# Optimization experiments

Measured on AMD Instinct MI355X. Metric: run time of the kernel, lower is better.

Reference implementation:

```python
import jax, jax.numpy as jnp
import numpy as np

N = 80000   # nodes
E = 320000  # directed edges
B = 3200    # graphs (25 nodes each)
D = 256     # emb_dim
L = 5       # num_layer
SIZES = [121, 8, 12, 15, 10, 9, 7, 3, 3]          # atom-feature vocab sizes
ESIZES = [25, 6, 2]                               # bond-feature vocab sizes
OFFS = np.concatenate([[0], np.cumsum(SIZES)[:-1]])  # offsets into fused node table
BN_EPS = 1e-5


def setup_inputs() -> dict:
    key = jax.random.key(0)
    ks = jax.random.split(key, 32)
    # int node features, per-column vocab bound
    x = jnp.stack([jax.random.randint(ks[i], (N,), 0, SIZES[i]) for i in range(9)], axis=1)
    edge_index = jax.random.randint(ks[9], (2, E), 0, N)
    edge_attr = jnp.stack([jax.random.randint(ks[10 + j], (E,), 0, ESIZES[j]) for j in range(3)], axis=1)
    batch = jnp.arange(N) // (N // B)  # sorted graph ids, 25 nodes per graph
    s = 0.1
    node_emb = jax.random.normal(ks[13], (int(sum(SIZES)), D)) * s  # fused 9 tables
    edge_emb1 = jax.random.normal(ks[14], (L, 25, D)) * s
    edge_emb2 = jax.random.normal(ks[15], (L, 6, D)) * s
    edge_emb3 = jax.random.normal(ks[16], (L, 2, D)) * s
    w = 0.05
    W1 = jax.random.normal(ks[17], (L, D, 2 * D)) * w
    b1 = jnp.zeros((L, 2 * D))
    W2 = jax.random.normal(ks[18], (L, 2 * D, D)) * w
    b2 = jnp.zeros((L, D))
    bn_g = jnp.ones((L, D))
    bn_b = jnp.zeros((L, D))
    H = D // 2
    HW1 = jax.random.normal(ks[19], (D, H)) * w
    Hb1 = jnp.zeros((H,))
    HW2 = jax.random.normal(ks[20], (H, H)) * w
    Hb2 = jnp.zeros((H,))
    HW3 = jax.random.normal(ks[21], (H, 2)) * w
    Hb3 = jnp.zeros((2,))
    return {"x": x, "edge_index": edge_index, "edge_attr": edge_attr, "batch": batch,
            "node_emb": node_emb, "edge_emb1": edge_emb1, "edge_emb2": edge_emb2,
            "edge_emb3": edge_emb3, "W1": W1, "b1": b1, "W2": W2, "b2": b2,
            "bn_g": bn_g, "bn_b": bn_b, "HW1": HW1, "Hb1": Hb1, "HW2": HW2,
            "Hb2": Hb2, "HW3": HW3, "Hb3": Hb3}


def _gnn_graphpred(x, edge_index, edge_attr, batch, node_emb, edge_emb1, edge_emb2,
                   edge_emb3, W1, b1, W2, b2, bn_g, bn_b, HW1, Hb1, HW2, Hb2, HW3, Hb3):
    n = x.shape[0]
    offs = jnp.asarray(OFFS, dtype=x.dtype)
    # sum of 9 atom embeddings == one gather into fused table
    h = node_emb[x + offs[None, :]].sum(axis=1)            # [N, D]
    # add self loops; self-loop edge_attr = [22, 0, 0]
    loop = jnp.arange(n, dtype=edge_index.dtype)
    src = jnp.concatenate([edge_index[0], loop])
    dst = jnp.concatenate([edge_index[1], loop])
    ea0 = jnp.concatenate([edge_attr[:, 0], jnp.full((n,), 22, edge_attr.dtype)])
    ea1 = jnp.concatenate([edge_attr[:, 1], jnp.zeros((n,), edge_attr.dtype)])
    ea2 = jnp.concatenate([edge_attr[:, 2], jnp.zeros((n,), edge_attr.dtype)])
    nl = W1.shape[0]
    relu_flag = jnp.arange(nl) < (nl - 1)   # ReLU on all but last layer (JK='last')

    def layer(hc, p):
        e1, e2, e3, w1, bb1, w2, bb2, g, b, flag = p
        eemb = e1[ea0] + e2[ea1] + e3[ea2]                 # [E+N, D]
        msg = hc[src] + eemb                                # gather + add
        aggr = jax.ops.segment_sum(msg, dst, num_segments=n)  # scatter-sum
        h2 = jax.nn.relu(aggr @ w1 + bb1) @ w2 + bb2        # GIN MLP
        mean = h2.mean(axis=0)
        var = h2.var(axis=0)                                # BatchNorm (batch stats)
        h2 = (h2 - mean) * jax.lax.rsqrt(var + BN_EPS) * g + b
        h2 = jnp.where(flag, jax.nn.relu(h2), h2)
        return h2, None

    h, _ = jax.lax.scan(layer, h, (edge_emb1, edge_emb2, edge_emb3, W1, b1, W2, b2,
                                   bn_g, bn_b, relu_flag))
    # super_node_rep: last node of each graph (batch is sorted)
    last_idx = jax.ops.segment_max(jnp.arange(n), batch, num_segments=B)
    super_rep = h[last_idx]                                 # [B, D]
    z = jax.nn.elu(super_rep @ HW1 + Hb1)
    z = jax.nn.elu(z @ HW2 + Hb2)
    return z @ HW3 + Hb3                                    # [B, 2]


def reference(x, edge_index, edge_attr, batch, node_emb, edge_emb1, edge_emb2,
              edge_emb3, W1, b1, W2, b2, bn_g, bn_b, HW1, Hb1, HW2, Hb2, HW3, Hb3):
    return _gnn_graphpred(x, edge_index, edge_attr, batch, node_emb, edge_emb1,
                          edge_emb2, edge_emb3, W1, b1, W2, b2, bn_g, bn_b,
                          HW1, Hb1, HW2, Hb2, HW3, Hb3)
```

## Files before the change

kernel.cpp:

```cpp
#include <hip/hip_runtime.h>
#include <hip/hip_bf16.h>

#define NN 80000
#define EE 320000
#define ET 400000
#define BB 3200
#define LL 5
#define NBLK 313

typedef __attribute__((ext_vector_type(8))) short bf16x8;
typedef __attribute__((ext_vector_type(8))) unsigned short u16x8;
typedef __attribute__((ext_vector_type(4))) float f32x4;

__device__ __forceinline__ float bf2f(unsigned short u) {
    unsigned int v = ((unsigned int)u) << 16;
    return __builtin_bit_cast(float, v);
}
__device__ __forceinline__ unsigned short f2bf(float f) {
    return __builtin_bit_cast(unsigned short, __float2bfloat16(f));
}


__global__ void k_deg(const int* ei, int* deg) {
    int e = blockIdx.x * 256 + threadIdx.x;
    if (e >= ET) return;
    int d = (e < EE) ? ei[EE + e] : (e - EE);
    atomicAdd(&deg[d], 1);
}

__global__ void k_scan1(const int* deg, int* blksum) {
    __shared__ int sh[256];
    int t = threadIdx.x, b = blockIdx.x;
    int i = b * 256 + t;
    int v = (i < NN) ? deg[i] : 0;
    sh[t] = v; __syncthreads();
    for (int off = 128; off > 0; off >>= 1) {
        if (t < off) sh[t] += sh[t + off];
        __syncthreads();
    }
    if (t == 0) blksum[b] = sh[0];
}

__global__ __launch_bounds__(512) void k_scan2(const int* blksum, int* blkoff) {
    __shared__ int sh[512];
    int t = threadIdx.x;
    int v = (t < NBLK) ? blksum[t] : 0;
    sh[t] = v; __syncthreads();
    for (int off = 1; off < 512; off <<= 1) {
        int x = (t >= off) ? sh[t - off] : 0;
        __syncthreads();
        sh[t] += x;
        __syncthreads();
    }
    if (t < NBLK) blkoff[t] = sh[t] - v;
}

__global__ void k_scan3(const int* deg, const int* blkoff, int* row_start, int* cursor) {
    __shared__ int sh[256];
    int t = threadIdx.x, b = blockIdx.x;
    int i = b * 256 + t;
    int v = (i < NN) ? deg[i] : 0;
    sh[t] = v; __syncthreads();
    for (int off = 1; off < 256; off <<= 1) {
        int x = (t >= off) ? sh[t - off] : 0;
        __syncthreads();
        sh[t] += x;
        __syncthreads();
    }
    int exc = sh[t] - v + blkoff[b];
    if (i < NN) { row_start[i] = exc; cursor[i] = exc; }
    if (i == NN - 1) row_start[NN] = exc + v;
}

__global__ void k_fill(const int* ei, const int* ea, int* cursor, int* eid, int* combo) {
    int e = blockIdx.x * 256 + threadIdx.x;
    if (e >= ET) return;
    int d = (e < EE) ? ei[EE + e] : (e - EE);
    int p = atomicAdd(&cursor[d], 1);
    eid[p] = e;
    int c;
    if (e < EE) c = ea[e * 3 + 0] * 12 + ea[e * 3 + 1] * 2 + ea[e * 3 + 2];
    else        c = 22 * 12;
    combo[e] = c;
}

__global__ void k_sortbkt(const int* row_start, int* eid) {
    int v = blockIdx.x * 256 + threadIdx.x;
    if (v >= NN) return;
    int s0 = row_start[v], s1 = row_start[v + 1];
    for (int i = s0 + 1; i < s1; i++) {
        int key = eid[i];
        int j = i - 1;
        while (j >= s0 && eid[j] > key) { eid[j + 1] = eid[j]; j--; }
        eid[j + 1] = key;
    }
}

__global__ void k_remap(const int* eid, const int* combo, const int* ei_src,
                        int* csrc, int* ccomb) {
    int p = blockIdx.x * 256 + threadIdx.x;
    if (p >= ET) return;
    int e = eid[p];
    csrc[p]  = (e < EE) ? ei_src[e] : (e - EE);
    ccomb[p] = combo[e];
}

__global__ void k_ecomb(const float* e1, const float* e2, const float* e3, float* ec) {
    int l = blockIdx.x / 300, c = blockIdx.x % 300, d = threadIdx.x;
    int a0 = c / 12, a1 = (c / 2) % 6, a2 = c & 1;
    ec[(size_t)(l * 300 + c) * 256 + d] =
        e1[(size_t)(l * 25 + a0) * 256 + d] +
        e2[(size_t)(l * 6 + a1) * 256 + d] +
        e3[(size_t)(l * 2 + a2) * 256 + d];
}

__global__ void k_w1t(const float* W, __hip_bfloat16* Wt) {
    int i = blockIdx.x * 256 + threadIdx.x;
    if (i >= LL * 512 * 256) return;
    int l = i / (512 * 256); int r = i % (512 * 256); int n = r / 256; int k = r % 256;
    Wt[i] = __float2bfloat16(W[(size_t)(l * 256 + k) * 512 + n]);
}
__global__ void k_w2t(const float* W, __hip_bfloat16* Wt) {
    int i = blockIdx.x * 256 + threadIdx.x;
    if (i >= LL * 256 * 512) return;
    int l = i / (256 * 512); int r = i % (256 * 512); int n = r / 512; int k = r % 512;
    Wt[i] = __float2bfloat16(W[(size_t)(l * 512 + k) * 256 + n]);
}

__global__ void k_nodeemb(const int* x, const float* emb, __hip_bfloat16* h) {
    const int offs[9] = {0, 121, 129, 141, 156, 166, 175, 182, 185};
    int i = blockIdx.x; int d = threadIdx.x;
    float acc = 0.f;
#pragma unroll
    for (int c = 0; c < 9; c++) {
        int idx = x[i * 9 + c] + offs[c];
        acc += emb[(size_t)idx * 256 + d];
    }
    h[(size_t)i * 256 + d] = __float2bfloat16(acc);
}


__global__ __launch_bounds__(256) void k_aggr(const __hip_bfloat16* h, const float* ecomb_l,
        const int* row_start, const int* csrc, const int* ccomb,
        __hip_bfloat16* aggrB) {
    int wid = threadIdx.x >> 6;
    int lane = threadIdx.x & 63;
    int v = blockIdx.x * 8 + wid * 2 + (lane >> 5);
    int sl = lane & 31;
    int s0 = row_start[v], s1 = row_start[v + 1];
    const unsigned short* hp = (const unsigned short*)h;
    float acc[8] = {0.f, 0.f, 0.f, 0.f, 0.f, 0.f, 0.f, 0.f};
    for (int p = s0; p < s1; p++) {
        int s = csrc[p];
        int c = ccomb[p];
        u16x8 hv = *(const u16x8*)(hp + (size_t)s * 256 + sl * 8);
        f32x4 e0 = *(const f32x4*)(ecomb_l + (size_t)c * 256 + sl * 8);
        f32x4 e1 = *(const f32x4*)(ecomb_l + (size_t)c * 256 + sl * 8 + 4);
        acc[0] += bf2f(hv[0]) + e0.x;
        acc[1] += bf2f(hv[1]) + e0.y;
        acc[2] += bf2f(hv[2]) + e0.z;
        acc[3] += bf2f(hv[3]) + e0.w;
        acc[4] += bf2f(hv[4]) + e1.x;
        acc[5] += bf2f(hv[5]) + e1.y;
        acc[6] += bf2f(hv[6]) + e1.z;
        acc[7] += bf2f(hv[7]) + e1.w;
    }
    u16x8 o;
#pragma unroll
    for (int j = 0; j < 8; j++) o[j] = f2bf(acc[j]);
    *(u16x8*)((unsigned short*)aggrB + (size_t)v * 256 + sl * 8) = o;
}

template<int K, bool RELU, bool OUTBF, bool STATS>
__global__ __launch_bounds__(256) void k_gemm(const __hip_bfloat16* A, const __hip_bfloat16* Wt,
                                              const float* bias, void* out, int Nn,
                                              float* psum, float* psq) {
    __shared__ short lA[2][128 * 32];
    __shared__ short lB[2][128 * 32];
    __shared__ float redS[4][64], redQ[4][64];
    int tid = threadIdx.x;
    int wave = tid >> 6, lane = tid & 63;
    int mBase = blockIdx.x * 128;
    int nBase = blockIdx.y * 128;
    int wr = (wave >> 1) * 64;
    int wc = (wave & 1) * 64;
    int lr = lane & 15, lk = lane >> 4;
    const short* Ap = (const short*)A + (size_t)mBase * K;
    const short* Bp = (const short*)Wt + (size_t)nBase * K;
    int srow = lane >> 2;
    int sslot = lane & 3;
    f32x4 acc[4][4] = {};
    constexpr int NT = K / 32;

    auto stage = [&](int buf, int k0) {
#pragma unroll
        for (int i = 0; i < 2; i++) {
            int chunk = wave * 2 + i;
            int r = chunk * 16 + srow;
            int scol = (sslot ^ ((r ^ (r >> 2)) & 3)) * 8;
            __builtin_amdgcn_global_load_lds(
                (const __attribute__((address_space(1))) unsigned int*)(Ap + (size_t)r * K + k0 + scol),
                (__attribute__((address_space(3))) unsigned int*)(&lA[buf][chunk * 512]), 16, 0, 0);
            __builtin_amdgcn_global_load_lds(
                (const __attribute__((address_space(1))) unsigned int*)(Bp + (size_t)r * K + k0 + scol),
                (__attribute__((address_space(3))) unsigned int*)(&lB[buf][chunk * 512]), 16, 0, 0);
        }
    };

    stage(0, 0);
    __syncthreads();

    for (int t = 0; t < NT; t++) {
        int cur = t & 1;
        if (t + 1 < NT) stage(cur ^ 1, (t + 1) * 32);
        bf16x8 a[4], b[4];
#pragma unroll
        for (int m = 0; m < 4; m++) {
            int r = wr + m * 16 + lr;
            a[m] = *(const bf16x8*)(&lA[cur][r * 32 + ((lk ^ ((r ^ (r >> 2)) & 3)) << 3)]);
        }
#pragma unroll
        for (int n = 0; n < 4; n++) {
            int r = wc + n * 16 + lr;
            b[n] = *(const bf16x8*)(&lB[cur][r * 32 + ((lk ^ ((r ^ (r >> 2)) & 3)) << 3)]);
        }
#pragma unroll
        for (int m = 0; m < 4; m++)
#pragma unroll
            for (int n = 0; n < 4; n++)
                acc[m][n] = __builtin_amdgcn_mfma_f32_16x16x32_bf16(a[m], b[n], acc[m][n], 0, 0, 0);
        __syncthreads();
    }

    float colS[4] = {0.f, 0.f, 0.f, 0.f}, colQ[4] = {0.f, 0.f, 0.f, 0.f};
#pragma unroll
    for (int m = 0; m < 4; m++)
#pragma unroll
        for (int n = 0; n < 4; n++) {
            int cdx = nBase + wc + n * 16 + lr;
            float bi = bias[cdx];
#pragma unroll
            for (int j = 0; j < 4; j++) {
                int r = mBase + wr + m * 16 + lk * 4 + j;
                float v = acc[m][n][j] + bi;
                if (RELU) v = fmaxf(v, 0.f);
                if (OUTBF) ((__hip_bfloat16*)out)[(size_t)r * Nn + cdx] = __float2bfloat16(v);
                else       ((float*)out)[(size_t)r * Nn + cdx] = v;
                if (STATS) { colS[n] += v; colQ[n] += v * v; }
            }
        }

    if (STATS) {
#pragma unroll
        for (int n = 0; n < 4; n++) {
            for (int off = 16; off < 64; off <<= 1) {
                colS[n] += __shfl_xor(colS[n], off);
                colQ[n] += __shfl_xor(colQ[n], off);
            }
        }
        if (lk == 0) {
#pragma unroll
            for (int n = 0; n < 4; n++) {
                redS[wave][n * 16 + lr] = colS[n];
                redQ[wave][n * 16 + lr] = colQ[n];
            }
        }
        __syncthreads();
        if (tid < 128) {
            int c = tid;
            int w0 = (c < 64) ? 0 : 1;
            int cc = c & 63;
            float S = redS[w0][cc] + redS[w0 + 2][cc];
            float Q = redQ[w0][cc] + redQ[w0 + 2][cc];
            psum[(size_t)(nBase + c) * 625 + blockIdx.x] = S;
            psq [(size_t)(nBase + c) * 625 + blockIdx.x] = Q;
        }
    }
}

__global__ __launch_bounds__(256) void k_bn2(const float* psum, const float* psq,
                                             const float* g, const float* bta, float* stat) {
    __shared__ float s1[256], s2[256];
    int d = blockIdx.x; int t = threadIdx.x;
    float a = 0.f, b = 0.f;
    for (int rb = t; rb < 625; rb += 256) {
        a += psum[(size_t)d * 625 + rb];
        b += psq [(size_t)d * 625 + rb];
    }
    s1[t] = a; s2[t] = b; __syncthreads();
    for (int off = 128; off > 0; off >>= 1) {
        if (t < off) { s1[t] += s1[t + off]; s2[t] += s2[t + off]; }
        __syncthreads();
    }
    if (t == 0) {
        float mean = s1[0] / NN;
        float var = s2[0] / NN - mean * mean;
        float sc = rsqrtf(var + 1e-5f) * g[d];
        stat[d] = sc;
        stat[256 + d] = bta[d] - mean * sc;
    }
}

__global__ void k_bnapply(const float* h2, const float* stat, __hip_bfloat16* h, int relu) {
    int i = (blockIdx.x * 256 + threadIdx.x) * 4;
    int d = i & 255;
    f32x4 v = *(const f32x4*)(h2 + i);
    f32x4 sc = *(const f32x4*)(stat + d);
    f32x4 sh = *(const f32x4*)(stat + 256 + d);
    float r0 = v.x * sc.x + sh.x;
    float r1 = v.y * sc.y + sh.y;
    float r2 = v.z * sc.z + sh.z;
    float r3 = v.w * sc.w + sh.w;
    if (relu) {
        r0 = fmaxf(r0, 0.f); r1 = fmaxf(r1, 0.f);
        r2 = fmaxf(r2, 0.f); r3 = fmaxf(r3, 0.f);
    }
    ushort4 o;
    o.x = f2bf(r0); o.y = f2bf(r1); o.z = f2bf(r2); o.w = f2bf(r3);
    *(ushort4*)((unsigned short*)h + i) = o;
}

__global__ __launch_bounds__(128) void k_head(const float* h2, const float* stat,
        const float* HW1, const float* Hb1, const float* HW2, const float* Hb2,
        const float* HW3, const float* Hb3, float* out) {
    __shared__ float row[256], z1[128], z2[128];
    int g = blockIdx.x; int t = threadIdx.x;
    size_t node = (size_t)g * 25 + 24;
    row[t]       = h2[node * 256 + t] * stat[t] + stat[256 + t];
    row[t + 128] = h2[node * 256 + t + 128] * stat[t + 128] + stat[256 + t + 128];
    __syncthreads();
    float acc = Hb1[t];
    for (int k = 0; k < 256; k++) acc += row[k] * HW1[k * 128 + t];
    z1[t] = acc > 0.f ? acc : expm1f(acc);
    __syncthreads();
    acc = Hb2[t];
    for (int k = 0; k < 128; k++) acc += z1[k] * HW2[k * 128 + t];
    z2[t] = acc > 0.f ? acc : expm1f(acc);
    __syncthreads();
    if (t < 2) {
        acc = Hb3[t];
        for (int k = 0; k < 128; k++) acc += z2[k] * HW3[k * 2 + t];
        out[g * 2 + t] = acc;
    }
}


extern "C" void kernel_launch(void* const* d_in, const int* in_sizes, int n_in,
                              void* d_out, int out_size, void* d_ws, size_t ws_size,
                              hipStream_t stream) {
    const int* x          = (const int*)d_in[0];
    const int* edge_index = (const int*)d_in[1];
    const int* edge_attr  = (const int*)d_in[2];
    const float* node_emb = (const float*)d_in[4];
    const float* ee1 = (const float*)d_in[5];
    const float* ee2 = (const float*)d_in[6];
    const float* ee3 = (const float*)d_in[7];
    const float* W1  = (const float*)d_in[8];
    const float* b1  = (const float*)d_in[9];
    const float* W2  = (const float*)d_in[10];
    const float* b2  = (const float*)d_in[11];
    const float* bng = (const float*)d_in[12];
    const float* bnb = (const float*)d_in[13];
    const float* HW1 = (const float*)d_in[14];
    const float* Hb1 = (const float*)d_in[15];
    const float* HW2 = (const float*)d_in[16];
    const float* Hb2 = (const float*)d_in[17];
    const float* HW3 = (const float*)d_in[18];
    const float* Hb3 = (const float*)d_in[19];
    float* out = (float*)d_out;

    char* ws = (char*)d_ws;
    size_t off = 0;
    auto alloc = [&](size_t bytes) -> char* {
        off = (off + 255) & ~(size_t)255;
        char* p = ws + off;
        off += bytes;
        return p;
    };
    int* deg       = (int*)alloc((size_t)NN * 4);
    int* cursor    = (int*)alloc((size_t)NN * 4);
    int* row_start = (int*)alloc((size_t)(NN + 1) * 4);
    int* blksum    = (int*)alloc((size_t)(NBLK + 1) * 4);
    int* blkoff    = (int*)alloc((size_t)(NBLK + 1) * 4);
    int* eid       = (int*)alloc((size_t)ET * 4);
    int* combo     = (int*)alloc((size_t)ET * 4);
    int* csrc      = (int*)alloc((size_t)ET * 4);
    int* ccomb     = (int*)alloc((size_t)ET * 4);
    float* ecomb   = (float*)alloc((size_t)LL * 300 * 256 * 4);
    __hip_bfloat16* W1t = (__hip_bfloat16*)alloc((size_t)LL * 512 * 256 * 2);
    __hip_bfloat16* W2t = (__hip_bfloat16*)alloc((size_t)LL * 256 * 512 * 2);
    __hip_bfloat16* h    = (__hip_bfloat16*)alloc((size_t)NN * 256 * 2);
    __hip_bfloat16* aggrB = (__hip_bfloat16*)alloc((size_t)NN * 256 * 2);
    __hip_bfloat16* act  = (__hip_bfloat16*)alloc((size_t)NN * 512 * 2);
    float* h2     = (float*)alloc((size_t)NN * 256 * 4);
    float* psum   = (float*)alloc((size_t)256 * 625 * 4);
    float* psq    = (float*)alloc((size_t)256 * 625 * 4);
    float* bnstat = (float*)alloc((size_t)512 * 4);

    hipMemsetAsync(deg, 0, (size_t)NN * 4, stream);
    k_deg<<<(ET + 255) / 256, 256, 0, stream>>>(edge_index, deg);
    k_scan1<<<NBLK, 256, 0, stream>>>(deg, blksum);
    k_scan2<<<1, 512, 0, stream>>>(blksum, blkoff);
    k_scan3<<<NBLK, 256, 0, stream>>>(deg, blkoff, row_start, cursor);
    k_fill<<<(ET + 255) / 256, 256, 0, stream>>>(edge_index, edge_attr, cursor, eid, combo);
    k_sortbkt<<<(NN + 255) / 256, 256, 0, stream>>>(row_start, eid);
    k_remap<<<(ET + 255) / 256, 256, 0, stream>>>(eid, combo, edge_index, csrc, ccomb);
    k_ecomb<<<LL * 300, 256, 0, stream>>>(ee1, ee2, ee3, ecomb);
    k_w1t<<<(LL * 512 * 256 + 255) / 256, 256, 0, stream>>>(W1, W1t);
    k_w2t<<<(LL * 256 * 512 + 255) / 256, 256, 0, stream>>>(W2, W2t);
    k_nodeemb<<<NN, 256, 0, stream>>>(x, node_emb, h);

    for (int l = 0; l < LL; l++) {
        k_aggr<<<NN / 8, 256, 0, stream>>>(h, ecomb + (size_t)l * 300 * 256, row_start,
                                           csrc, ccomb, aggrB);
        k_gemm<256, true, true, false><<<dim3(625, 4), 256, 0, stream>>>(
            aggrB, W1t + (size_t)l * 512 * 256, b1 + l * 512, act, 512, nullptr, nullptr);
        k_gemm<512, false, false, true><<<dim3(625, 2), 256, 0, stream>>>(
            act, W2t + (size_t)l * 256 * 512, b2 + l * 256, h2, 256, psum, psq);
        k_bn2<<<256, 256, 0, stream>>>(psum, psq, bng + l * 256, bnb + l * 256, bnstat);
        if (l < LL - 1)
            k_bnapply<<<NN * 256 / (256 * 4), 256, 0, stream>>>(h2, bnstat, h, 1);
    }

    k_head<<<BB, 128, 0, stream>>>(h2, bnstat, HW1, Hb1, HW2, Hb2, HW3, Hb3, out);
}
```

Baseline: 944.3 us.

## Fuse GIN MLP GEMMs into one kernel with split-bf16 weights

Replaces the two separate GEMM launches per layer with one kernel. Each block computes a 64-row tile of the first GEMM and keeps the ReLU activation in swizzled LDS, then runs the second GEMM from LDS, so the 512-wide activation no longer round-trips through global memory. Weights are split into bf16 hi and lo parts, which doubles the MFMA count to recover fp32-like weight precision. The B operands are now read directly from global memory without LDS staging, which may cost bandwidth. The last layer writes h2 only for the rows the head reads.

```diff
diff --git a/kernel.cpp b/kernel.cpp
--- a/kernel.cpp
+++ b/kernel.cpp
@@ -7,6 +7,7 @@
 #define BB 3200
 #define LL 5
 #define NBLK 313
+#define MLPB 1250
 
 typedef __attribute__((ext_vector_type(8))) short bf16x8;
 typedef __attribute__((ext_vector_type(8))) unsigned short u16x8;
@@ -114,17 +115,23 @@
         e3[(size_t)(l * 2 + a2) * 256 + d];
 }
 
-__global__ void k_w1t(const float* W, __hip_bfloat16* Wt) {
+__global__ void k_w1t(const float* W, __hip_bfloat16* Whi, __hip_bfloat16* Wlo) {
     int i = blockIdx.x * 256 + threadIdx.x;
     if (i >= LL * 512 * 256) return;
     int l = i / (512 * 256); int r = i % (512 * 256); int n = r / 256; int k = r % 256;
-    Wt[i] = __float2bfloat16(W[(size_t)(l * 256 + k) * 512 + n]);
-}
-__global__ void k_w2t(const float* W, __hip_bfloat16* Wt) {
+    float w = W[(size_t)(l * 256 + k) * 512 + n];
+    unsigned short hi = f2bf(w);
+    Whi[i] = __float2bfloat16(w);
+    Wlo[i] = __float2bfloat16(w - bf2f(hi));
+}
+__global__ void k_w2t(const float* W, __hip_bfloat16* Whi, __hip_bfloat16* Wlo) {
     int i = blockIdx.x * 256 + threadIdx.x;
     if (i >= LL * 256 * 512) return;
     int l = i / (256 * 512); int r = i % (256 * 512); int n = r / 512; int k = r % 512;
-    Wt[i] = __float2bfloat16(W[(size_t)(l * 512 + k) * 256 + n]);
+    float w = W[(size_t)(l * 512 + k) * 256 + n];
+    unsigned short hi = f2bf(w);
+    Whi[i] = __float2bfloat16(w);
+    Wlo[i] = __float2bfloat16(w - bf2f(hi));
 }
 
 __global__ void k_nodeemb(const int* x, const float* emb, __hip_bfloat16* h) {
@@ -171,109 +178,112 @@
     *(u16x8*)((unsigned short*)aggrB + (size_t)v * 256 + sl * 8) = o;
 }
 
-template<int K, bool RELU, bool OUTBF, bool STATS>
-__global__ __launch_bounds__(256) void k_gemm(const __hip_bfloat16* A, const __hip_bfloat16* Wt,
-                                              const float* bias, void* out, int Nn,
-                                              float* psum, float* psq) {
-    __shared__ short lA[2][128 * 32];
-    __shared__ short lB[2][128 * 32];
-    __shared__ float redS[4][64], redQ[4][64];
+template<bool LAST>
+__global__ __launch_bounds__(512) void k_mlp(const __hip_bfloat16* aggrB,
+        const __hip_bfloat16* W1hi, const __hip_bfloat16* W1lo, const float* b1v,
+        const __hip_bfloat16* W2hi, const __hip_bfloat16* W2lo, const float* b2v,
+        float* h2, float* psum, float* psq) {
+    __shared__ short sAct[64 * 512];
     int tid = threadIdx.x;
     int wave = tid >> 6, lane = tid & 63;
-    int mBase = blockIdx.x * 128;
-    int nBase = blockIdx.y * 128;
-    int wr = (wave >> 1) * 64;
-    int wc = (wave & 1) * 64;
     int lr = lane & 15, lk = lane >> 4;
-    const short* Ap = (const short*)A + (size_t)mBase * K;
-    const short* Bp = (const short*)Wt + (size_t)nBase * K;
-    int srow = lane >> 2;
-    int sslot = lane & 3;
-    f32x4 acc[4][4] = {};
-    constexpr int NT = K / 32;
-
-    auto stage = [&](int buf, int k0) {
-#pragma unroll
-        for (int i = 0; i < 2; i++) {
-            int chunk = wave * 2 + i;
-            int r = chunk * 16 + srow;
-            int scol = (sslot ^ ((r ^ (r >> 2)) & 3)) * 8;
-            __builtin_amdgcn_global_load_lds(
-                (const __attribute__((address_space(1))) unsigned int*)(Ap + (size_t)r * K + k0 + scol),
-                (__attribute__((address_space(3))) unsigned int*)(&lA[buf][chunk * 512]), 16, 0, 0);
-            __builtin_amdgcn_global_load_lds(
-                (const __attribute__((address_space(1))) unsigned int*)(Bp + (size_t)r * K + k0 + scol),
-                (__attribute__((address_space(3))) unsigned int*)(&lB[buf][chunk * 512]), 16, 0, 0);
-        }
-    };
-
-    stage(0, 0);
+    int mBase = blockIdx.x * 64;
+
+    const short* Ap  = (const short*)aggrB + (size_t)mBase * 256;
+    const short* B1h = (const short*)W1hi + (size_t)(wave * 64) * 256;
+    const short* B1l = (const short*)W1lo + (size_t)(wave * 64) * 256;
+    f32x4 acc1[4][4] = {};
+#pragma unroll 1
+    for (int t = 0; t < 8; t++) {
+        int k0 = t * 32;
+        bf16x8 a[4], bh[4], bl[4];
+#pragma unroll
+        for (int m = 0; m < 4; m++)
+            a[m] = *(const bf16x8*)(Ap + (size_t)(m * 16 + lr) * 256 + k0 + lk * 8);
+#pragma unroll
+        for (int n = 0; n < 4; n++) {
+            bh[n] = *(const bf16x8*)(B1h + (size_t)(n * 16 + lr) * 256 + k0 + lk * 8);
+            bl[n] = *(const bf16x8*)(B1l + (size_t)(n * 16 + lr) * 256 + k0 + lk * 8);
+        }
+#pragma unroll
+        for (int m = 0; m < 4; m++)
+#pragma unroll
+            for (int n = 0; n < 4; n++) {
+                acc1[m][n] = __builtin_amdgcn_mfma_f32_16x16x32_bf16(a[m], bh[n], acc1[m][n], 0, 0, 0);
+                acc1[m][n] = __builtin_amdgcn_mfma_f32_16x16x32_bf16(a[m], bl[n], acc1[m][n], 0, 0, 0);
+            }
+    }
+#pragma unroll
+    for (int m = 0; m < 4; m++)
+#pragma unroll
+        for (int n = 0; n < 4; n++) {
+            int col = wave * 64 + n * 16 + lr;
+            float bi = b1v[col];
+            int cb = col >> 3, ci = col & 7;
+#pragma unroll
+            for (int j = 0; j < 4; j++) {
+                int row = m * 16 + lk * 4 + j;
+                float v = fmaxf(acc1[m][n][j] + bi, 0.f);
+                sAct[row * 512 + ((cb ^ (row & 7)) << 3) + ci] = (short)f2bf(v);
+            }
+        }
     __syncthreads();
 
-    for (int t = 0; t < NT; t++) {
-        int cur = t & 1;
-        if (t + 1 < NT) stage(cur ^ 1, (t + 1) * 32);
-        bf16x8 a[4], b[4];
+    const short* B2h = (const short*)W2hi + (size_t)(wave * 32) * 512;
+    const short* B2l = (const short*)W2lo + (size_t)(wave * 32) * 512;
+    f32x4 acc2[4][2] = {};
+#pragma unroll 1
+    for (int t = 0; t < 16; t++) {
+        int kb = t * 4 + lk;
+        bf16x8 a2[4], b2h[2], b2l[2];
 #pragma unroll
         for (int m = 0; m < 4; m++) {
-            int r = wr + m * 16 + lr;
-            a[m] = *(const bf16x8*)(&lA[cur][r * 32 + ((lk ^ ((r ^ (r >> 2)) & 3)) << 3)]);
-        }
-#pragma unroll
-        for (int n = 0; n < 4; n++) {
-            int r = wc + n * 16 + lr;
-            b[n] = *(const bf16x8*)(&lB[cur][r * 32 + ((lk ^ ((r ^ (r >> 2)) & 3)) << 3)]);
+            int row = m * 16 + lr;
+            a2[m] = *(const bf16x8*)(&sAct[row * 512 + ((kb ^ (row & 7)) << 3)]);
+        }
+#pragma unroll
+        for (int n = 0; n < 2; n++) {
+            b2h[n] = *(const bf16x8*)(B2h + (size_t)(n * 16 + lr) * 512 + t * 32 + lk * 8);
+            b2l[n] = *(const bf16x8*)(B2l + (size_t)(n * 16 + lr) * 512 + t * 32 + lk * 8);
         }
 #pragma unroll
         for (int m = 0; m < 4; m++)
 #pragma unroll
-            for (int n = 0; n < 4; n++)
-                acc[m][n] = __builtin_amdgcn_mfma_f32_16x16x32_bf16(a[m], b[n], acc[m][n], 0, 0, 0);
-        __syncthreads();
-    }
-
-    float colS[4] = {0.f, 0.f, 0.f, 0.f}, colQ[4] = {0.f, 0.f, 0.f, 0.f};
+            for (int n = 0; n < 2; n++) {
+                acc2[m][n] = __builtin_amdgcn_mfma_f32_16x16x32_bf16(a2[m], b2h[n], acc2[m][n], 0, 0, 0);
+                acc2[m][n] = __builtin_amdgcn_mfma_f32_16x16x32_bf16(a2[m], b2l[n], acc2[m][n], 0, 0, 0);
+            }
+    }
+
+    float colS[2] = {0.f, 0.f}, colQ[2] = {0.f, 0.f};
 #pragma unroll
     for (int m = 0; m < 4; m++)
 #pragma unroll
-        for (int n = 0; n < 4; n++) {
-            int cdx = nBase + wc + n * 16 + lr;
-            float bi = bias[cdx];
+        for (int n = 0; n < 2; n++) {
+            int col = wave * 32 + n * 16 + lr;
+            float bi = b2v[col];
 #pragma unroll
             for (int j = 0; j < 4; j++) {
-                int r = mBase + wr + m * 16 + lk * 4 + j;
-                float v = acc[m][n][j] + bi;
-                if (RELU) v = fmaxf(v, 0.f);
-                if (OUTBF) ((__hip_bfloat16*)out)[(size_t)r * Nn + cdx] = __float2bfloat16(v);
-                else       ((float*)out)[(size_t)r * Nn + cdx] = v;
-                if (STATS) { colS[n] += v; colQ[n] += v * v; }
+                int row = mBase + m * 16 + lk * 4 + j;
+                float v = acc2[m][n][j] + bi;
+                colS[n] += v; colQ[n] += v * v;
+                if (!LAST || (row % 25 == 24))
+                    h2[(size_t)row * 256 + col] = v;
             }
         }
-
-    if (STATS) {
-#pragma unroll
-        for (int n = 0; n < 4; n++) {
-            for (int off = 16; off < 64; off <<= 1) {
-                colS[n] += __shfl_xor(colS[n], off);
-                colQ[n] += __shfl_xor(colQ[n], off);
-            }
-        }
-        if (lk == 0) {
-#pragma unroll
-            for (int n = 0; n < 4; n++) {
-                redS[wave][n * 16 + lr] = colS[n];
-                redQ[wave][n * 16 + lr] = colQ[n];
-            }
-        }
-        __syncthreads();
-        if (tid < 128) {
-            int c = tid;
-            int w0 = (c < 64) ? 0 : 1;
-            int cc = c & 63;
-            float S = redS[w0][cc] + redS[w0 + 2][cc];
-            float Q = redQ[w0][cc] + redQ[w0 + 2][cc];
-            psum[(size_t)(nBase + c) * 625 + blockIdx.x] = S;
-            psq [(size_t)(nBase + c) * 625 + blockIdx.x] = Q;
+#pragma unroll
+    for (int n = 0; n < 2; n++) {
+        colS[n] += __shfl_xor(colS[n], 16);
+        colQ[n] += __shfl_xor(colQ[n], 16);
+        colS[n] += __shfl_xor(colS[n], 32);
+        colQ[n] += __shfl_xor(colQ[n], 32);
+    }
+    if (lk == 0) {
+#pragma unroll
+        for (int n = 0; n < 2; n++) {
+            int col = wave * 32 + n * 16 + lr;
+            psum[(size_t)col * MLPB + blockIdx.x] = colS[n];
+            psq [(size_t)col * MLPB + blockIdx.x] = colQ[n];
         }
     }
 }
@@ -283,9 +293,9 @@
     __shared__ float s1[256], s2[256];
     int d = blockIdx.x; int t = threadIdx.x;
     float a = 0.f, b = 0.f;
-    for (int rb = t; rb < 625; rb += 256) {
-        a += psum[(size_t)d * 625 + rb];
-        b += psq [(size_t)d * 625 + rb];
+    for (int rb = t; rb < MLPB; rb += 256) {
+        a += psum[(size_t)d * MLPB + rb];
+        b += psq [(size_t)d * MLPB + rb];
     }
     s1[t] = a; s2[t] = b; __syncthreads();
     for (int off = 128; off > 0; off >>= 1) {
@@ -387,14 +397,15 @@
     int* csrc      = (int*)alloc((size_t)ET * 4);
     int* ccomb     = (int*)alloc((size_t)ET * 4);
     float* ecomb   = (float*)alloc((size_t)LL * 300 * 256 * 4);
-    __hip_bfloat16* W1t = (__hip_bfloat16*)alloc((size_t)LL * 512 * 256 * 2);
-    __hip_bfloat16* W2t = (__hip_bfloat16*)alloc((size_t)LL * 256 * 512 * 2);
+    __hip_bfloat16* W1hi = (__hip_bfloat16*)alloc((size_t)LL * 512 * 256 * 2);
+    __hip_bfloat16* W1lo = (__hip_bfloat16*)alloc((size_t)LL * 512 * 256 * 2);
+    __hip_bfloat16* W2hi = (__hip_bfloat16*)alloc((size_t)LL * 256 * 512 * 2);
+    __hip_bfloat16* W2lo = (__hip_bfloat16*)alloc((size_t)LL * 256 * 512 * 2);
     __hip_bfloat16* h    = (__hip_bfloat16*)alloc((size_t)NN * 256 * 2);
     __hip_bfloat16* aggrB = (__hip_bfloat16*)alloc((size_t)NN * 256 * 2);
-    __hip_bfloat16* act  = (__hip_bfloat16*)alloc((size_t)NN * 512 * 2);
     float* h2     = (float*)alloc((size_t)NN * 256 * 4);
-    float* psum   = (float*)alloc((size_t)256 * 625 * 4);
-    float* psq    = (float*)alloc((size_t)256 * 625 * 4);
+    float* psum   = (float*)alloc((size_t)256 * MLPB * 4);
+    float* psq    = (float*)alloc((size_t)256 * MLPB * 4);
     float* bnstat = (float*)alloc((size_t)512 * 4);
 
     hipMemsetAsync(deg, 0, (size_t)NN * 4, stream);
@@ -406,17 +417,24 @@
     k_sortbkt<<<(NN + 255) / 256, 256, 0, stream>>>(row_start, eid);
     k_remap<<<(ET + 255) / 256, 256, 0, stream>>>(eid, combo, edge_index, csrc, ccomb);
     k_ecomb<<<LL * 300, 256, 0, stream>>>(ee1, ee2, ee3, ecomb);
-    k_w1t<<<(LL * 512 * 256 + 255) / 256, 256, 0, stream>>>(W1, W1t);
-    k_w2t<<<(LL * 256 * 512 + 255) / 256, 256, 0, stream>>>(W2, W2t);
+    k_w1t<<<(LL * 512 * 256 + 255) / 256, 256, 0, stream>>>(W1, W1hi, W1lo);
+    k_w2t<<<(LL * 256 * 512 + 255) / 256, 256, 0, stream>>>(W2, W2hi, W2lo);
     k_nodeemb<<<NN, 256, 0, stream>>>(x, node_emb, h);
 
     for (int l = 0; l < LL; l++) {
         k_aggr<<<NN / 8, 256, 0, stream>>>(h, ecomb + (size_t)l * 300 * 256, row_start,
                                            csrc, ccomb, aggrB);
-        k_gemm<256, true, true, false><<<dim3(625, 4), 256, 0, stream>>>(
-            aggrB, W1t + (size_t)l * 512 * 256, b1 + l * 512, act, 512, nullptr, nullptr);
-        k_gemm<512, false, false, true><<<dim3(625, 2), 256, 0, stream>>>(
-            act, W2t + (size_t)l * 256 * 512, b2 + l * 256, h2, 256, psum, psq);
+        if (l < LL - 1) {
+            k_mlp<false><<<MLPB, 512, 0, stream>>>(aggrB,
+                W1hi + (size_t)l * 512 * 256, W1lo + (size_t)l * 512 * 256, b1 + l * 512,
+                W2hi + (size_t)l * 256 * 512, W2lo + (size_t)l * 256 * 512, b2 + l * 256,
+                h2, psum, psq);
+        } else {
+            k_mlp<true><<<MLPB, 512, 0, stream>>>(aggrB,
+                W1hi + (size_t)l * 512 * 256, W1lo + (size_t)l * 512 * 256, b1 + l * 512,
+                W2hi + (size_t)l * 256 * 512, W2lo + (size_t)l * 256 * 512, b2 + l * 256,
+                h2, psum, psq);
+        }
         k_bn2<<<256, 256, 0, stream>>>(psum, psq, bng + l * 256, bnb + l * 256, bnstat);
         if (l < LL - 1)
             k_bnapply<<<NN * 256 / (256 * 4), 256, 0, stream>>>(h2, bnstat, h, 1);
```

Result: slower. 1.393 ms (+47.5%).
